# Kernel optimization log

Measured on AMD Instinct MI355X. Metric: run time of the kernel, lower is better.

## Reference

```python
import jax, jax.numpy as jnp
import numpy as np
from jax.scipy.special import gammaln

N_I = 100000
N_J = 100000
D = 8
S_I = 6000
S_J = 6000
NNZ = 500000
EPS = 1e-06


def setup_inputs() -> dict:
    key = jax.random.key(0)
    ks = jax.random.split(key, 9)
    beta = jax.random.normal(ks[0], (N_I,), dtype=jnp.float32)
    gamma = jax.random.normal(ks[1], (N_J,), dtype=jnp.float32)
    latent_zi = jax.random.normal(ks[2], (N_I, D), dtype=jnp.float32)
    latent_zj = jax.random.normal(ks[3], (N_J, D), dtype=jnp.float32)
    # multinomial-without-replacement node samples -> random permutation prefix
    sample_i_idx = jax.random.permutation(ks[4], N_I)[:S_I]
    sample_j_idx = jax.random.permutation(ks[5], N_J)[:S_J]
    # spspmm-selected subgraph links (global node indices) with edge counts
    sparse_i_sample = jax.random.randint(ks[6], (NNZ,), 0, N_I)
    sparse_j_sample = jax.random.randint(ks[7], (NNZ,), 0, N_J)
    valueC = jax.random.uniform(ks[8], (NNZ,), dtype=jnp.float32)
    return {
        'beta': beta, 'gamma': gamma,
        'latent_zi': latent_zi, 'latent_zj': latent_zj,
        'valueC': valueC,
        'sample_i_idx': sample_i_idx, 'sample_j_idx': sample_j_idx,
        'sparse_i_sample': sparse_i_sample, 'sparse_j_sample': sparse_j_sample,
    }


def reference(beta, gamma, latent_zi, latent_zj, valueC,
              sample_i_idx, sample_j_idx, sparse_i_sample, sparse_j_sample):
    # Dense non-link term over sampled (I, J) block
    zi = latent_zi[sample_i_idx]            # [S_I, D]
    zj = latent_zj[sample_j_idx]            # [S_J, D]
    diff = zi[:, None, :] - zj[None, :, :] + EPS   # [S_I, S_J, D]
    z_dist = jnp.sqrt(jnp.sum(diff * diff, axis=-1))  # [S_I, S_J]
    Lambda = beta[sample_i_idx][:, None] + gamma[sample_j_idx][None, :] - z_dist
    # Sparse link terms (Poisson log-likelihood)
    dl = latent_zi[sparse_i_sample] - latent_zj[sparse_j_sample] + EPS  # [NNZ, D]
    z_dist_links = jnp.sqrt(jnp.sum(dl * dl, axis=-1))                  # [NNZ]
    bias_links = beta[sparse_i_sample] + gamma[sparse_j_sample]
    log_Lambda_links = valueC * (bias_links - z_dist_links)
    LL = jnp.sum(log_Lambda_links - gammaln(valueC + 1.0)) - jnp.sum(jnp.exp(Lambda))
    return LL
```

## Files before the change

kernel.cpp:

```cpp
#include <hip/hip_runtime.h>
#include <math.h>

#define NI_TOT 100000
#define NJ_TOT 100000
#define DD 8
#define SI_N 6000
#define SJ_N 6000
#define NNZ_N 500000
#define EPSF 1e-6f
#define LOG2E 1.44269504088896f
#define INV_LOG2E 0.693147180559945f

#define TI 64
#define JPT 4
#define JTILE (256 * JPT)
#define ND_I ((SI_N + TI - 1) / TI)
#define NJT ((SJ_N + JTILE - 1) / JTILE)
#define N_DENSE_BLOCKS (ND_I * NJT)
#define LPT 4
#define SPARSE_SPAN (256 * LPT)
#define N_SPARSE_BLOCKS ((NNZ_N + SPARSE_SPAN - 1) / SPARSE_SPAN)
#define N_TOTAL_BLOCKS (N_DENSE_BLOCKS + N_SPARSE_BLOCKS)

#define GA1 (-0.577191652f)
#define GA2 ( 0.988205891f)
#define GA3 (-0.897056937f)
#define GA4 ( 0.918206857f)
#define GA5 (-0.756704078f)
#define GA6 ( 0.482199394f)
#define GA7 (-0.193527818f)
#define GA8 ( 0.035868343f)

__global__ __launch_bounds__(256) void fused_kernel(
    const float* __restrict__ beta, const float* __restrict__ gamma,
    const float* __restrict__ zi_all, const float* __restrict__ zj_all,
    const float* __restrict__ valueC,
    const int* __restrict__ si, const int* __restrict__ sj,
    const int* __restrict__ spi, const int* __restrict__ spj,
    float* __restrict__ partials, float* __restrict__ out, int mode)
{
    __shared__ float sRed[4];
    __shared__ __align__(16) float  sZi[TI * DD];
    __shared__ __align__(8)  float2 sIB[TI];

    const int t = threadIdx.x;
    float blocksum = 0.0f;

    if (blockIdx.x < N_DENSE_BLOCKS) {
        const int it = blockIdx.x % ND_I;
        const int js = blockIdx.x / ND_I;
        const int i0 = it * TI;

        for (int idx = t; idx < TI * DD; idx += 256) {
            int r = idx >> 3, d = idx & 7;
            int gi = i0 + r;
            float v = (gi < SI_N) ? zi_all[(size_t)si[gi] * DD + d] : 0.0f;
            sZi[idx] = (v + EPSF) * (-2.0f * LOG2E);
        }
        __syncthreads();
        if (t < TI) {
            int gi = i0 + t;
            float s = 0.0f;
#pragma unroll
            for (int d = 0; d < DD; ++d) {
                float m = sZi[t * DD + d];
                s = fmaf(m, m, s);
            }
            float eb = 0.0f;
            if (gi < SI_N) eb = __builtin_amdgcn_exp2f(beta[si[gi]] * LOG2E);
            sIB[t] = make_float2(0.25f * s, eb);
        }

        const int jb = js * JTILE + t * JPT;
        float zc[JPT][DD], s2[JPT], gf[JPT];
#pragma unroll
        for (int u = 0; u < JPT; ++u) {
            int gj = jb + u;
            if (gj < SJ_N) {
                int row = sj[gj];
                const float4* q = (const float4*)(zj_all + (size_t)row * DD);
                float4 q0 = q[0], q1 = q[1];
                zc[u][0]=q0.x*LOG2E; zc[u][1]=q0.y*LOG2E; zc[u][2]=q0.z*LOG2E; zc[u][3]=q0.w*LOG2E;
                zc[u][4]=q1.x*LOG2E; zc[u][5]=q1.y*LOG2E; zc[u][6]=q1.z*LOG2E; zc[u][7]=q1.w*LOG2E;
                gf[u] = __builtin_amdgcn_exp2f(gamma[row] * LOG2E);
            } else {
#pragma unroll
                for (int d = 0; d < DD; ++d) zc[u][d] = 0.0f;
                gf[u] = 0.0f;
            }
            float s = 0.0f;
#pragma unroll
            for (int d = 0; d < DD; ++d) s = fmaf(zc[u][d], zc[u][d], s);
            s2[u] = s;
        }
        __syncthreads();

        float acc[JPT] = {0.0f, 0.0f, 0.0f, 0.0f};
        float4 cr0 = *(const float4*)&sZi[0];
        float4 cr1 = *(const float4*)&sZi[4];
        float2 cib = sIB[0];
#pragma unroll 4
        for (int a = 0; a < TI; ++a) {
            float4 nr0, nr1; float2 nib;
            if (a + 1 < TI) {
                nr0 = *(const float4*)&sZi[(a + 1) * DD];
                nr1 = *(const float4*)&sZi[(a + 1) * DD + 4];
                nib = sIB[a + 1];
            }
#pragma unroll
            for (int u = 0; u < JPT; ++u) {
                float dd;
                dd = fmaf(cr0.x, zc[u][0], cib.x);
                dd = fmaf(cr0.y, zc[u][1], dd);
                dd = fmaf(cr0.z, zc[u][2], dd);
                dd = fmaf(cr0.w, zc[u][3], dd);
                dd = fmaf(cr1.x, zc[u][4], dd);
                dd = fmaf(cr1.y, zc[u][5], dd);
                dd = fmaf(cr1.z, zc[u][6], dd);
                dd = fmaf(cr1.w, zc[u][7], dd);
                float ss = fmaxf(dd + s2[u], 1e-20f);
                float dist = __builtin_amdgcn_sqrtf(ss);
                float e = __builtin_amdgcn_exp2f(-dist);
                acc[u] = fmaf(cib.y, e, acc[u]);
            }
            cr0 = nr0; cr1 = nr1; cib = nib;
        }
        float bs = 0.0f;
#pragma unroll
        for (int u = 0; u < JPT; ++u) bs = fmaf(gf[u], acc[u], bs);
        blocksum = -bs;
    } else {
        const int base = (blockIdx.x - N_DENSE_BLOCKS) * SPARSE_SPAN + t;
        float val = 0.0f;
#pragma unroll
        for (int u = 0; u < LPT; ++u) {
            const int idx = base + u * 256;
            if (idx < NNZ_N) {
                const int i = spi[idx], j = spj[idx];
                const float c = valueC[idx];
                const float4* zi4 = (const float4*)(zi_all + (size_t)i * DD);
                const float4* zj4 = (const float4*)(zj_all + (size_t)j * DD);
                float4 a0 = zi4[0], a1 = zi4[1];
                float4 b0 = zj4[0], b1 = zj4[1];
                float ss = 0.0f, df;
                df = a0.x-b0.x+EPSF; ss = fmaf(df,df,ss);
                df = a0.y-b0.y+EPSF; ss = fmaf(df,df,ss);
                df = a0.z-b0.z+EPSF; ss = fmaf(df,df,ss);
                df = a0.w-b0.w+EPSF; ss = fmaf(df,df,ss);
                df = a1.x-b1.x+EPSF; ss = fmaf(df,df,ss);
                df = a1.y-b1.y+EPSF; ss = fmaf(df,df,ss);
                df = a1.z-b1.z+EPSF; ss = fmaf(df,df,ss);
                df = a1.w-b1.w+EPSF; ss = fmaf(df,df,ss);
                ss = fmaxf(ss, 1e-20f);
                float dist = __builtin_amdgcn_sqrtf(ss);
                float bg = beta[i] + gamma[j];
                float g = 1.0f + c*(GA1 + c*(GA2 + c*(GA3 + c*(GA4 + c*(GA5
                              + c*(GA6 + c*(GA7 + c*GA8)))))));
                val += c * (bg - dist) - __builtin_amdgcn_logf(g) * INV_LOG2E;
            }
        }
        blocksum = val;
    }

    float acc = blocksum;
#pragma unroll
    for (int off = 32; off; off >>= 1) acc += __shfl_down(acc, off, 64);
    const int lane = t & 63, w = t >> 6;
    if (lane == 0) sRed[w] = acc;
    __syncthreads();
    if (t == 0) {
        float s = sRed[0] + sRed[1] + sRed[2] + sRed[3];
        if (mode) atomicAdd(out, s);
        else partials[blockIdx.x] = s;
    }
}

__global__ __launch_bounds__(256) void final_reduce_kernel(
    const float* __restrict__ p, int n, float* __restrict__ out)
{
    __shared__ float sRed[4];
    float s = 0.0f;
    for (int i = threadIdx.x; i < n; i += 256) s += p[i];
#pragma unroll
    for (int off = 32; off; off >>= 1) s += __shfl_down(s, off, 64);
    const int lane = threadIdx.x & 63, w = threadIdx.x >> 6;
    if (lane == 0) sRed[w] = s;
    __syncthreads();
    if (threadIdx.x == 0) out[0] = sRed[0] + sRed[1] + sRed[2] + sRed[3];
}

extern "C" void kernel_launch(void* const* d_in, const int* in_sizes, int n_in,
                              void* d_out, int out_size, void* d_ws, size_t ws_size,
                              hipStream_t stream) {
    const float* beta   = (const float*)d_in[0];
    const float* gamma  = (const float*)d_in[1];
    const float* zi     = (const float*)d_in[2];
    const float* zj     = (const float*)d_in[3];
    const float* valueC = (const float*)d_in[4];
    const int* si   = (const int*)d_in[5];
    const int* sjx  = (const int*)d_in[6];
    const int* spi  = (const int*)d_in[7];
    const int* spj  = (const int*)d_in[8];
    float* out = (float*)d_out;

    const int ntot = N_TOTAL_BLOCKS;
    const size_t need = (size_t)ntot * sizeof(float);

    if (d_ws && ws_size >= need) {
        float* p = (float*)d_ws;
        fused_kernel<<<ntot, 256, 0, stream>>>(
            beta, gamma, zi, zj, valueC, si, sjx, spi, spj, p, out, 0);
        final_reduce_kernel<<<1, 256, 0, stream>>>(p, ntot, out);
    } else {
        hipMemsetAsync(out, 0, sizeof(float), stream);
        fused_kernel<<<ntot, 256, 0, stream>>>(
            beta, gamma, zi, zj, valueC, si, sjx, spi, spj, nullptr, out, 1);
    }
}
```

Measured before the change: 113.8 us.

## Pack latent rows to fp16 for sparse gathers and reorder sparse blocks first

A new pre-pass kernel converts both latent matrices and the bias vectors into fp16 buffers in the workspace, so each sparse-link gather reads 16 bytes per row instead of 32. Sparse blocks now come before dense blocks in the grid. The per-block partials array and final reduce kernel are replaced by atomicAdd into an output zeroed by the pack kernel. This trades the extra pack pass over all 200k rows (about 10 MB read) and a loss of precision in the link terms for cheaper random gathers.

```diff
diff --git a/kernel.cpp b/kernel.cpp
--- a/kernel.cpp
+++ b/kernel.cpp
@@ -1,4 +1,5 @@
 #include <hip/hip_runtime.h>
+#include <hip/hip_fp16.h>
 #include <math.h>
 
 #define NI_TOT 100000
@@ -22,6 +23,11 @@
 #define N_SPARSE_BLOCKS ((NNZ_N + SPARSE_SPAN - 1) / SPARSE_SPAN)
 #define N_TOTAL_BLOCKS (N_DENSE_BLOCKS + N_SPARSE_BLOCKS)
 
+#define NROWS (NI_TOT + NJ_TOT)
+#define HZ_BYTES ((size_t)NROWS * DD * 2)
+#define HB_BYTES ((size_t)NROWS * 2)
+#define WS_NEED (HZ_BYTES + HB_BYTES)
+
 #define GA1 (-0.577191652f)
 #define GA2 ( 0.988205891f)
 #define GA3 (-0.897056937f)
@@ -31,13 +37,49 @@
 #define GA7 (-0.193527818f)
 #define GA8 ( 0.035868343f)
 
+__global__ __launch_bounds__(256) void pack_kernel(
+    const float* __restrict__ beta, const float* __restrict__ gamma,
+    const float* __restrict__ zi_all, const float* __restrict__ zj_all,
+    __half* __restrict__ hz, __half* __restrict__ hb, float* __restrict__ out)
+{
+    const int r = blockIdx.x * 256 + threadIdx.x;
+    if (r == 0) out[0] = 0.0f;
+    if (r < NROWS) {
+        const float* src = (r < NI_TOT) ? zi_all + (size_t)r * DD
+                                        : zj_all + (size_t)(r - NI_TOT) * DD;
+        float4 a = ((const float4*)src)[0];
+        float4 b = ((const float4*)src)[1];
+        __half2 h0 = __floats2half2_rn(a.x, a.y);
+        __half2 h1 = __floats2half2_rn(a.z, a.w);
+        __half2 h2 = __floats2half2_rn(b.x, b.y);
+        __half2 h3 = __floats2half2_rn(b.z, b.w);
+        uint4 u;
+        u.x = *(unsigned*)&h0; u.y = *(unsigned*)&h1;
+        u.z = *(unsigned*)&h2; u.w = *(unsigned*)&h3;
+        ((uint4*)hz)[r] = u;
+    } else if (r < 2 * NROWS) {
+        const int q = r - NROWS;
+        float v = (q < NI_TOT) ? beta[q] : gamma[q - NI_TOT];
+        hb[q] = __float2half(v);
+    }
+}
+
+__device__ __forceinline__ void unpack_row(uint4 u, float f[DD]) {
+    float2 p;
+    p = __half22float2(*(__half2*)&u.x); f[0] = p.x; f[1] = p.y;
+    p = __half22float2(*(__half2*)&u.y); f[2] = p.x; f[3] = p.y;
+    p = __half22float2(*(__half2*)&u.z); f[4] = p.x; f[5] = p.y;
+    p = __half22float2(*(__half2*)&u.w); f[6] = p.x; f[7] = p.y;
+}
+
 __global__ __launch_bounds__(256) void fused_kernel(
     const float* __restrict__ beta, const float* __restrict__ gamma,
     const float* __restrict__ zi_all, const float* __restrict__ zj_all,
     const float* __restrict__ valueC,
     const int* __restrict__ si, const int* __restrict__ sj,
     const int* __restrict__ spi, const int* __restrict__ spj,
-    float* __restrict__ partials, float* __restrict__ out, int mode)
+    const __half* __restrict__ hz, const __half* __restrict__ hb,
+    float* __restrict__ out, int mode)
 {
     __shared__ float sRed[4];
     __shared__ __align__(16) float  sZi[TI * DD];
@@ -46,9 +88,10 @@
     const int t = threadIdx.x;
     float blocksum = 0.0f;
 
-    if (blockIdx.x < N_DENSE_BLOCKS) {
-        const int it = blockIdx.x % ND_I;
-        const int js = blockIdx.x / ND_I;
+    if (blockIdx.x >= N_SPARSE_BLOCKS) {
+        const int db = blockIdx.x - N_SPARSE_BLOCKS;
+        const int it = db % ND_I;
+        const int js = db / ND_I;
         const int i0 = it * TI;
 
         for (int idx = t; idx < TI * DD; idx += 256) {
@@ -130,14 +173,32 @@
         for (int u = 0; u < JPT; ++u) bs = fmaf(gf[u], acc[u], bs);
         blocksum = -bs;
     } else {
-        const int base = (blockIdx.x - N_DENSE_BLOCKS) * SPARSE_SPAN + t;
+        const int base = blockIdx.x * SPARSE_SPAN + t;
         float val = 0.0f;
+        const uint4* hzv = (const uint4*)hz;
 #pragma unroll
         for (int u = 0; u < LPT; ++u) {
             const int idx = base + u * 256;
-            if (idx < NNZ_N) {
-                const int i = spi[idx], j = spj[idx];
-                const float c = valueC[idx];
+            if (idx >= NNZ_N) continue;
+            const int i = spi[idx], j = spj[idx];
+            const float c = valueC[idx];
+            float dist, bg;
+            if (mode == 0) {
+                uint4 ui = hzv[i];
+                uint4 uj = hzv[NI_TOT + j];
+                float fi[DD], fj[DD];
+                unpack_row(ui, fi);
+                unpack_row(uj, fj);
+                float ss = 0.0f;
+#pragma unroll
+                for (int d = 0; d < DD; ++d) {
+                    float df = fi[d] - fj[d] + EPSF;
+                    ss = fmaf(df, df, ss);
+                }
+                ss = fmaxf(ss, 1e-20f);
+                dist = __builtin_amdgcn_sqrtf(ss);
+                bg = __half2float(hb[i]) + __half2float(hb[NI_TOT + j]);
+            } else {
                 const float4* zi4 = (const float4*)(zi_all + (size_t)i * DD);
                 const float4* zj4 = (const float4*)(zj_all + (size_t)j * DD);
                 float4 a0 = zi4[0], a1 = zi4[1];
@@ -152,12 +213,12 @@
                 df = a1.z-b1.z+EPSF; ss = fmaf(df,df,ss);
                 df = a1.w-b1.w+EPSF; ss = fmaf(df,df,ss);
                 ss = fmaxf(ss, 1e-20f);
-                float dist = __builtin_amdgcn_sqrtf(ss);
-                float bg = beta[i] + gamma[j];
-                float g = 1.0f + c*(GA1 + c*(GA2 + c*(GA3 + c*(GA4 + c*(GA5
-                              + c*(GA6 + c*(GA7 + c*GA8)))))));
-                val += c * (bg - dist) - __builtin_amdgcn_logf(g) * INV_LOG2E;
-            }
+                dist = __builtin_amdgcn_sqrtf(ss);
+                bg = beta[i] + gamma[j];
+            }
+            float g = 1.0f + c*(GA1 + c*(GA2 + c*(GA3 + c*(GA4 + c*(GA5
+                          + c*(GA6 + c*(GA7 + c*GA8)))))));
+            val += c * (bg - dist) - __builtin_amdgcn_logf(g) * INV_LOG2E;
         }
         blocksum = val;
     }
@@ -170,23 +231,8 @@
     __syncthreads();
     if (t == 0) {
         float s = sRed[0] + sRed[1] + sRed[2] + sRed[3];
-        if (mode) atomicAdd(out, s);
-        else partials[blockIdx.x] = s;
-    }
-}
-
-__global__ __launch_bounds__(256) void final_reduce_kernel(
-    const float* __restrict__ p, int n, float* __restrict__ out)
-{
-    __shared__ float sRed[4];
-    float s = 0.0f;
-    for (int i = threadIdx.x; i < n; i += 256) s += p[i];
-#pragma unroll
-    for (int off = 32; off; off >>= 1) s += __shfl_down(s, off, 64);
-    const int lane = threadIdx.x & 63, w = threadIdx.x >> 6;
-    if (lane == 0) sRed[w] = s;
-    __syncthreads();
-    if (threadIdx.x == 0) out[0] = sRed[0] + sRed[1] + sRed[2] + sRed[3];
+        atomicAdd(out, s);
+    }
 }
 
 extern "C" void kernel_launch(void* const* d_in, const int* in_sizes, int n_in,
@@ -203,17 +249,17 @@
     const int* spj  = (const int*)d_in[8];
     float* out = (float*)d_out;
 
-    const int ntot = N_TOTAL_BLOCKS;
-    const size_t need = (size_t)ntot * sizeof(float);
-
-    if (d_ws && ws_size >= need) {
-        float* p = (float*)d_ws;
-        fused_kernel<<<ntot, 256, 0, stream>>>(
-            beta, gamma, zi, zj, valueC, si, sjx, spi, spj, p, out, 0);
-        final_reduce_kernel<<<1, 256, 0, stream>>>(p, ntot, out);
+    if (d_ws && ws_size >= WS_NEED) {
+        __half* hz = (__half*)d_ws;
+        __half* hb = (__half*)((char*)d_ws + HZ_BYTES);
+        const int packb = (2 * NROWS + 255) / 256;
+        pack_kernel<<<packb, 256, 0, stream>>>(beta, gamma, zi, zj, hz, hb, out);
+        fused_kernel<<<N_TOTAL_BLOCKS, 256, 0, stream>>>(
+            beta, gamma, zi, zj, valueC, si, sjx, spi, spj, hz, hb, out, 0);
     } else {
         hipMemsetAsync(out, 0, sizeof(float), stream);
-        fused_kernel<<<ntot, 256, 0, stream>>>(
-            beta, gamma, zi, zj, valueC, si, sjx, spi, spj, nullptr, out, 1);
-    }
-}
+        fused_kernel<<<N_TOTAL_BLOCKS, 256, 0, stream>>>(
+            beta, gamma, zi, zj, valueC, si, sjx, spi, spj,
+            (const __half*)zi, (const __half*)zi, out, 1);
+    }
+}
```

After: 118.1 us. +3.8%, slower.
